# Kernel tuning notes

Hardware: AMD Instinct MI355X
Metric: run time of the kernel (lower is better)

The kernel has to match this reference:

```python
import jax, jax.numpy as jnp
import numpy as np

EPS = 1e-5


def setup_inputs() -> dict:
    key = jax.random.key(0)
    ks = jax.random.split(key, 6)
    B, C, H, W, K = 8, 512, 128, 128, 32
    x = jax.random.normal(ks[0], (B, C, H, W), jnp.float32)
    # 1x1 conv projection (ConvModule with BN -> no conv bias)
    conv_w = jax.random.normal(ks[1], (C, C), jnp.float32) * 0.02
    bn2_gamma = jnp.ones((C,), jnp.float32)
    bn2_beta = jnp.zeros((C,), jnp.float32)
    bn2_mean = jnp.zeros((C,), jnp.float32)
    bn2_var = jnp.ones((C,), jnp.float32)
    # Encoding: codewords [K, C], per-code smoothing scale [K]
    codewords = jax.random.normal(ks[2], (K, C), jnp.float32) * 0.1
    scale = -jax.random.uniform(ks[3], (K,), jnp.float32)  # negative scale as in mmcv init
    # BN1d over num_codes
    bn1_gamma = jnp.ones((K,), jnp.float32)
    bn1_beta = jnp.zeros((K,), jnp.float32)
    bn1_mean = jnp.zeros((K,), jnp.float32)
    bn1_var = jnp.ones((K,), jnp.float32)
    # channel-attention fc
    fc_w = jax.random.normal(ks[4], (C, C), jnp.float32) * 0.02
    fc_b = jnp.zeros((C,), jnp.float32)
    return {
        "x": x, "conv_w": conv_w,
        "bn2_gamma": bn2_gamma, "bn2_beta": bn2_beta, "bn2_mean": bn2_mean, "bn2_var": bn2_var,
        "codewords": codewords, "scale": scale,
        "bn1_gamma": bn1_gamma, "bn1_beta": bn1_beta, "bn1_mean": bn1_mean, "bn1_var": bn1_var,
        "fc_w": fc_w, "fc_b": fc_b,
    }


def reference(x, conv_w, bn2_gamma, bn2_beta, bn2_mean, bn2_var,
              codewords, scale, bn1_gamma, bn1_beta, bn1_mean, bn1_var,
              fc_w, fc_b):
    B, C, H, W = x.shape
    K = codewords.shape[0]
    # --- encoding_project: 1x1 conv + BN2d (eval) + ReLU ---
    p = jnp.einsum('bchw,oc->bohw', x, conv_w)
    inv2 = jax.lax.rsqrt(bn2_var + EPS)
    p = (p - bn2_mean[None, :, None, None]) * (inv2 * bn2_gamma)[None, :, None, None] \
        + bn2_beta[None, :, None, None]
    p = jax.nn.relu(p)
    # --- Encoding: scaled-L2 soft assignment + aggregation ---
    feat = p.reshape(B, C, H * W).transpose(0, 2, 1)          # [B, N, C]
    x2 = jnp.sum(feat * feat, axis=-1)                        # [B, N]
    c2 = jnp.sum(codewords * codewords, axis=-1)              # [K]
    xc = jnp.einsum('bnc,kc->bnk', feat, codewords)           # [B, N, K]
    scaled_l2 = scale[None, None, :] * (x2[:, :, None] - 2.0 * xc + c2[None, None, :])
    aw = jax.nn.softmax(scaled_l2, axis=2)                    # [B, N, K]
    # sum_n aw * (feat_n - c_k), without materializing [B,N,K,C]
    enc = jnp.einsum('bnk,bnc->bkc', aw, feat) \
        - jnp.sum(aw, axis=1)[:, :, None] * codewords[None]   # [B, K, C]
    # --- BN1d over codes (eval) + ReLU, then mean over codes ---
    inv1 = jax.lax.rsqrt(bn1_var + EPS)
    enc = (enc - bn1_mean[None, :, None]) * (inv1 * bn1_gamma)[None, :, None] \
        + bn1_beta[None, :, None]
    enc = jax.nn.relu(enc)
    encoding_feat = jnp.mean(enc, axis=1)                     # [B, C]
    # --- sigmoid channel gate + residual multiply-add + ReLU ---
    gamma = jax.nn.sigmoid(encoding_feat @ fc_w.T + fc_b)     # [B, C]
    output = jax.nn.relu(x + x * gamma[:, :, None, None])
    return (encoding_feat, output)
```

## Files before the change

kernel.cpp:

```cpp
#include <hip/hip_runtime.h>
#include <stdint.h>


#define EPSV 1e-5f

constexpr int Bn = 8, Cn = 512, Kn = 32, Nn = 16384;
constexpr int TILE_N = 64;
constexpr int NBLK = 256, BLK_PER_B = NBLK / Bn;
constexpr int TILES_PER_BLK = (Nn / TILE_N) / BLK_PER_B;

typedef float f32x4 __attribute__((ext_vector_type(4)));
typedef __bf16 bf16x8 __attribute__((ext_vector_type(8)));
union U4B8 { uint4 u; bf16x8 b; };

__device__ __forceinline__ uint32_t f2bf(float f) {
  uint32_t u = __float_as_uint(f);
  u += 0x7fffu + ((u >> 16) & 1u);
  return u >> 16;
}
__device__ __forceinline__ float bflo(uint32_t d) { return __uint_as_float(d << 16); }
__device__ __forceinline__ float bfhi(uint32_t d) { return __uint_as_float(d & 0xffff0000u); }

__global__ void k0_prep(const float* __restrict__ conv_w, const float* __restrict__ codewords,
                        const float* __restrict__ g2, const float* __restrict__ b2,
                        const float* __restrict__ m2, const float* __restrict__ v2,
                        uint16_t* __restrict__ WT2, uint16_t* __restrict__ cwb,
                        float* __restrict__ c2, float* __restrict__ bns, float* __restrict__ bnb)
{
  const int idx = blockIdx.x * blockDim.x + threadIdx.x;
  if (idx < Cn * Cn) {
    const int o = idx >> 9, c = idx & 511;
    const int cc = c >> 5, cl = c & 31;
    WT2[((size_t)cc * 512 + o) * 32 + cl] = (uint16_t)f2bf(conv_w[idx]);
  }
  if (idx < Kn * Cn) cwb[idx] = (uint16_t)f2bf(codewords[idx]);
  if (idx < Cn) {
    const float s = g2[idx] * rsqrtf(v2[idx] + EPSV);
    bns[idx] = s;
    bnb[idx] = b2[idx] - m2[idx] * s;
  }
  if (idx < Kn) {
    float s = 0.f;
    for (int c = 0; c < Cn; ++c) { const float v = codewords[idx * 512 + c]; s = fmaf(v, v, s); }
    c2[idx] = s;
  }
}

__launch_bounds__(512, 2)
__global__ void k1_main(const float* __restrict__ x,
                        const uint16_t* __restrict__ WT2,
                        const uint16_t* __restrict__ cwb,
                        const float* __restrict__ bns, const float* __restrict__ bnb,
                        const float* __restrict__ c2g, const float* __restrict__ scaleg,
                        float* __restrict__ encpart, float* __restrict__ awsumpart,
                        int parts)
{
  __shared__ __align__(16) uint32_t sP[512][33];
  __shared__ __align__(16) uint16_t sXF[64][520];
  __shared__ __align__(16) float    sAW[64][33];
  __shared__ float sX2[64];
  __shared__ float sBNs[512], sBNb[512];
  __shared__ float sScale[Kn], sC2[Kn];

  const int t    = threadIdx.x;
  const int lane = t & 63, w = t >> 6;
  const int col  = lane & 15, quad = lane >> 4;
  const int b    = blockIdx.x / BLK_PER_B;
  const int tb0  = blockIdx.x % BLK_PER_B;

  {
    sBNs[t] = bns[t];
    sBNb[t] = bnb[t];
    if (t < Kn) { sScale[t] = scaleg[t]; sC2[t] = c2g[t]; }
  }

  float enc[32];
#pragma unroll
  for (int u = 0; u < 32; ++u) enc[u] = 0.f;
  float awacc = 0.f;
  const int k_e3 = t & 31, cg = t >> 5;

  for (int j = 0; j < TILES_PER_BLK; ++j) {
    const int n0 = (tb0 + j * BLK_PER_B) * TILE_N;

    {
      const int c0 = t >> 4, n4 = (t & 15) * 4;
      const float* xp = x + ((size_t)(b * Cn) + c0) * Nn + n0 + n4;
      const int n2 = n4 >> 1;
#pragma unroll
      for (int i = 0; i < 16; ++i) {
        const float4 v = *(const float4*)(xp + (size_t)i * 32 * Nn);
        sP[c0 + i * 32][n2 + 0] = f2bf(v.x) | (f2bf(v.y) << 16);
        sP[c0 + i * 32][n2 + 1] = f2bf(v.z) | (f2bf(v.w) << 16);
      }
    }
    __syncthreads();

    {
      const int n = t & 63, seg = t >> 6;
      const int h = (n & 1) * 16, n2 = n >> 1;
#pragma unroll
      for (int u = 0; u < 8; ++u) {
        const int c0 = seg * 64 + u * 8;
        uint32_t o0, o1, o2, o3;
        {
          const uint32_t d0 = sP[c0 + 0][n2], d1 = sP[c0 + 1][n2];
          o0 = ((d0 >> h) & 0xffffu) | (((d1 >> h) & 0xffffu) << 16);
        }
        {
          const uint32_t d0 = sP[c0 + 2][n2], d1 = sP[c0 + 3][n2];
          o1 = ((d0 >> h) & 0xffffu) | (((d1 >> h) & 0xffffu) << 16);
        }
        {
          const uint32_t d0 = sP[c0 + 4][n2], d1 = sP[c0 + 5][n2];
          o2 = ((d0 >> h) & 0xffffu) | (((d1 >> h) & 0xffffu) << 16);
        }
        {
          const uint32_t d0 = sP[c0 + 6][n2], d1 = sP[c0 + 7][n2];
          o3 = ((d0 >> h) & 0xffffu) | (((d1 >> h) & 0xffffu) << 16);
        }
        *(uint4*)&sXF[n][c0] = make_uint4(o0, o1, o2, o3);
      }
    }
    __syncthreads();

    f32x4 acc[4][4];
#pragma unroll
    for (int ot = 0; ot < 4; ++ot)
#pragma unroll
      for (int nt = 0; nt < 4; ++nt) acc[ot][nt] = (f32x4){0.f, 0.f, 0.f, 0.f};

    {
      uint4 areg[2][4];
      const uint16_t* wbase = WT2 + (w * 64 + col) * 32 + quad * 8;
#pragma unroll
      for (int ot = 0; ot < 4; ++ot) areg[0][ot] = *(const uint4*)(wbase + ot * 512);
#pragma unroll
      for (int cc = 0; cc < 16; ++cc) {
        const int cur = cc & 1;
        if (cc + 1 < 16) {
          const uint16_t* wp = wbase + (size_t)(cc + 1) * 16384;
#pragma unroll
          for (int ot = 0; ot < 4; ++ot) areg[cur ^ 1][ot] = *(const uint4*)(wp + ot * 512);
        }
        U4B8 bfr[4];
#pragma unroll
        for (int nt = 0; nt < 4; ++nt)
          bfr[nt].u = *(const uint4*)&sXF[nt * 16 + col][cc * 32 + quad * 8];
#pragma unroll
        for (int ot = 0; ot < 4; ++ot) {
          U4B8 a; a.u = areg[cur][ot];
#pragma unroll
          for (int nt = 0; nt < 4; ++nt)
            acc[ot][nt] = __builtin_amdgcn_mfma_f32_16x16x32_bf16(a.b, bfr[nt].b, acc[ot][nt], 0, 0, 0);
        }
      }
    }
    __syncthreads();

#pragma unroll
    for (int ot = 0; ot < 4; ++ot) {
      const int ob = w * 64 + ot * 16 + quad * 4;
      const float4 s4 = *(const float4*)&sBNs[ob];
      const float4 b4 = *(const float4*)&sBNb[ob];
#pragma unroll
      for (int nt = 0; nt < 4; ++nt) {
        const f32x4 a = acc[ot][nt];
        const float r0 = fmaxf(fmaf(a[0], s4.x, b4.x), 0.f);
        const float r1 = fmaxf(fmaf(a[1], s4.y, b4.y), 0.f);
        const float r2 = fmaxf(fmaf(a[2], s4.z, b4.z), 0.f);
        const float r3 = fmaxf(fmaf(a[3], s4.w, b4.w), 0.f);
        *(uint2*)&sXF[nt * 16 + col][ob] = make_uint2(f2bf(r0) | (f2bf(r1) << 16),
                                                      f2bf(r2) | (f2bf(r3) << 16));
      }
    }
    __syncthreads();

    {
      const int n = t >> 3, cb = (t & 7) * 64;
      float s = 0.f;
#pragma unroll
      for (int u = 0; u < 8; ++u) {
        const uint4 d = *(const uint4*)&sXF[n][cb + u * 8];
        s = fmaf(bflo(d.x), bflo(d.x), s); s = fmaf(bfhi(d.x), bfhi(d.x), s);
        s = fmaf(bflo(d.y), bflo(d.y), s); s = fmaf(bfhi(d.y), bfhi(d.y), s);
        s = fmaf(bflo(d.z), bflo(d.z), s); s = fmaf(bfhi(d.z), bfhi(d.z), s);
        s = fmaf(bflo(d.w), bflo(d.w), s); s = fmaf(bfhi(d.w), bfhi(d.w), s);
      }
      s += __shfl_xor(s, 1); s += __shfl_xor(s, 2); s += __shfl_xor(s, 4);
      if ((t & 7) == 0) sX2[n] = s;
    }

    {
      const int kt = w & 1, ntl = w >> 1;
      f32x4 xca = (f32x4){0.f, 0.f, 0.f, 0.f};
      const uint16_t* cwp = cwb + (size_t)(kt * 16 + col) * 512 + quad * 8;
#pragma unroll
      for (int ks = 0; ks < 16; ++ks) {
        U4B8 af, bf;
        af.u = *(const uint4*)(cwp + ks * 32);
        bf.u = *(const uint4*)&sXF[ntl * 16 + col][ks * 32 + quad * 8];
        xca = __builtin_amdgcn_mfma_f32_16x16x32_bf16(af.b, bf.b, xca, 0, 0, 0);
      }
#pragma unroll
      for (int r = 0; r < 4; ++r)
        sAW[ntl * 16 + col][kt * 16 + quad * 4 + r] = xca[r];
    }
    __syncthreads();

    if (t < 64) {
      const float x2v = sX2[t];
      float m = -1e30f;
#pragma unroll
      for (int k = 0; k < Kn; ++k) {
        const float l = sScale[k] * (x2v - 2.f * sAW[t][k] + sC2[k]);
        sAW[t][k] = l;
        m = fmaxf(m, l);
      }
      float s = 0.f;
#pragma unroll
      for (int k = 0; k < Kn; ++k) { const float e = __expf(sAW[t][k] - m); sAW[t][k] = e; s += e; }
      const float inv = 1.f / s;
#pragma unroll
      for (int k = 0; k < Kn; ++k) sAW[t][k] *= inv;
    }
    __syncthreads();

#pragma unroll 2
    for (int n = 0; n < TILE_N; ++n) {
      const float a = sAW[n][k_e3];
      if (cg == 0) awacc += a;
      const uint16_t* fp = &sXF[n][cg * 32];
#pragma unroll
      for (int u = 0; u < 4; ++u) {
        const uint4 d = *(const uint4*)(fp + u * 8);
        enc[u*8+0] = fmaf(a, bflo(d.x), enc[u*8+0]);
        enc[u*8+1] = fmaf(a, bfhi(d.x), enc[u*8+1]);
        enc[u*8+2] = fmaf(a, bflo(d.y), enc[u*8+2]);
        enc[u*8+3] = fmaf(a, bfhi(d.y), enc[u*8+3]);
        enc[u*8+4] = fmaf(a, bflo(d.z), enc[u*8+4]);
        enc[u*8+5] = fmaf(a, bfhi(d.z), enc[u*8+5]);
        enc[u*8+6] = fmaf(a, bflo(d.w), enc[u*8+6]);
        enc[u*8+7] = fmaf(a, bfhi(d.w), enc[u*8+7]);
      }
    }
  }

  if (parts > 1) {
    float* dst = encpart + (((size_t)tb0 * Bn + b) * Kn + k_e3) * Cn + cg * 32;
#pragma unroll
    for (int u = 0; u < 8; ++u)
      *(float4*)(dst + u * 4) = make_float4(enc[u*4+0], enc[u*4+1], enc[u*4+2], enc[u*4+3]);
    if (cg == 0) awsumpart[((size_t)tb0 * Bn + b) * Kn + k_e3] = awacc;
  } else {
    float* dst = encpart + ((size_t)b * Kn + k_e3) * Cn + cg * 32;
#pragma unroll
    for (int u = 0; u < 32; ++u) atomicAdd(dst + u, enc[u]);
    if (cg == 0) atomicAdd(awsumpart + (size_t)b * Kn + k_e3, awacc);
  }
}

__global__ void k2a_reduce(float* __restrict__ encpart, int parts)
{
  const int b = blockIdx.x >> 5, s = blockIdx.x & 31;
  const int e0 = s * 512 + threadIdx.x;
#pragma unroll
  for (int r = 0; r < 2; ++r) {
    const size_t base = (size_t)b * (Kn * Cn) + e0 + r * 256;
    float v = encpart[base];
    for (int p = 1; p < parts; ++p)
      v += encpart[base + (size_t)p * (Bn * Kn * Cn)];
    encpart[base] = v;
  }
}

__global__ void k2_post(const float* __restrict__ encpart, const float* __restrict__ awsumpart,
                        const float* __restrict__ codewords,
                        const float* __restrict__ g1, const float* __restrict__ b1,
                        const float* __restrict__ m1, const float* __restrict__ v1,
                        const float* __restrict__ fc_w, const float* __restrict__ fc_b,
                        float* __restrict__ ef_out, float* __restrict__ gamma,
                        int parts)
{
  __shared__ float efs[Cn];
  __shared__ float saws[Kn];
  const int b = blockIdx.x, c = threadIdx.x;

  if (c < Kn) {
    float s = 0.f;
    for (int p = 0; p < parts; ++p) s += awsumpart[((size_t)p * Bn + b) * Kn + c];
    saws[c] = s;
  }
  __syncthreads();

  float s = 0.f;
#pragma unroll 4
  for (int k = 0; k < Kn; ++k) {
    float e = encpart[((size_t)b * Kn + k) * Cn + c] - saws[k] * codewords[k * Cn + c];
    const float inv = rsqrtf(v1[k] + EPSV);
    e = (e - m1[k]) * (inv * g1[k]) + b1[k];
    s += fmaxf(e, 0.f);
  }
  s *= (1.f / 32.f);
  efs[c] = s;
  ef_out[b * Cn + c] = s;
  __syncthreads();
  const float4* w4 = (const float4*)(fc_w + (size_t)c * Cn);
  const float4* e4 = (const float4*)efs;
  float z = 0.f;
#pragma unroll 8
  for (int i = 0; i < Cn / 4; ++i) {
    const float4 w = w4[i], e = e4[i];
    z = fmaf(w.x, e.x, z); z = fmaf(w.y, e.y, z);
    z = fmaf(w.z, e.z, z); z = fmaf(w.w, e.w, z);
  }
  z += fc_b[c];
  gamma[b * Cn + c] = 1.f / (1.f + __expf(-z));
}

__global__ void k3_out(const float* __restrict__ x, const float* __restrict__ gamma,
                       float* __restrict__ out)
{
  const float4* x4 = (const float4*)x;
  float4* o4 = (float4*)out;
  int i = blockIdx.x * blockDim.x + threadIdx.x;
#pragma unroll
  for (int r = 0; r < 8; ++r, i += 2097152) {
    const int bb = i >> 21;
    const int cc = (i >> 12) & 511;
    const float g = 1.f + gamma[bb * 512 + cc];
    float4 v = x4[i];
    v.x = fmaxf(v.x * g, 0.f);
    v.y = fmaxf(v.y * g, 0.f);
    v.z = fmaxf(v.z * g, 0.f);
    v.w = fmaxf(v.w * g, 0.f);
    o4[i] = v;
  }
}

extern "C" void kernel_launch(void* const* d_in, const int* in_sizes, int n_in,
                              void* d_out, int out_size, void* d_ws, size_t ws_size,
                              hipStream_t stream) {
  const float* x      = (const float*)d_in[0];
  const float* conv_w = (const float*)d_in[1];
  const float* bn2g   = (const float*)d_in[2];
  const float* bn2b   = (const float*)d_in[3];
  const float* bn2m   = (const float*)d_in[4];
  const float* bn2v   = (const float*)d_in[5];
  const float* codew  = (const float*)d_in[6];
  const float* scale  = (const float*)d_in[7];
  const float* bn1g   = (const float*)d_in[8];
  const float* bn1b   = (const float*)d_in[9];
  const float* bn1m   = (const float*)d_in[10];
  const float* bn1v   = (const float*)d_in[11];
  const float* fc_w   = (const float*)d_in[12];
  const float* fc_b   = (const float*)d_in[13];

  const size_t enc_part_bytes = (size_t)BLK_PER_B * Bn * Kn * Cn * 4;
  const size_t aws_part_bytes = (size_t)BLK_PER_B * Bn * Kn * 4;
  const size_t enc_fall_bytes = (size_t)Bn * Kn * Cn * 4;
  const size_t aws_fall_bytes = (size_t)Bn * Kn * 4;
  const size_t fixed_bytes = (size_t)Bn * Cn * 4
                           + (size_t)Cn * Cn * 2
                           + (size_t)Kn * Cn * 2
                           + (size_t)Kn * 4
                           + (size_t)Cn * 4
                           + (size_t)Cn * 4;
  const bool use_parts = ws_size >= enc_part_bytes + aws_part_bytes + fixed_bytes;
  const int parts = use_parts ? BLK_PER_B : 1;
  const size_t enc_bytes = use_parts ? enc_part_bytes : enc_fall_bytes;
  const size_t aws_bytes = use_parts ? aws_part_bytes : aws_fall_bytes;

  char* ws = (char*)d_ws;
  float*    encpart  = (float*)ws;                       ws += enc_bytes;
  float*    awsumpart= (float*)ws;                       ws += aws_bytes;
  float*    gamma    = (float*)ws;                       ws += (size_t)Bn * Cn * 4;
  uint16_t* WT2      = (uint16_t*)ws;                    ws += (size_t)Cn * Cn * 2;
  uint16_t* cwb      = (uint16_t*)ws;                    ws += (size_t)Kn * Cn * 2;
  float*    c2       = (float*)ws;                       ws += (size_t)Kn * 4;
  float*    bns      = (float*)ws;                       ws += (size_t)Cn * 4;
  float*    bnb      = (float*)ws;

  if (!use_parts)
    hipMemsetAsync(encpart, 0, enc_bytes + aws_bytes, stream);

  k0_prep<<<1024, 256, 0, stream>>>(conv_w, codew, bn2g, bn2b, bn2m, bn2v,
                                    WT2, cwb, c2, bns, bnb);
  k1_main<<<NBLK, 512, 0, stream>>>(x, WT2, cwb, bns, bnb, c2, scale,
                                    encpart, awsumpart, parts);
  if (parts > 1)
    k2a_reduce<<<256, 256, 0, stream>>>(encpart, parts);
  k2_post<<<Bn, Cn, 0, stream>>>(encpart, awsumpart, codew, bn1g, bn1b, bn1m, bn1v,
                                 fc_w, fc_b, (float*)d_out, gamma, parts);
  k3_out<<<8192, 256, 0, stream>>>(x, gamma, (float*)d_out + Bn * Cn);
}
```

Before: 999.1 us.

## Drop staging LDS buffer, load x directly transposed, raise occupancy and grid size

Removes the sP staging buffer and its second transpose pass: each thread now reads scalar x values along N for four channels and writes packed bf16 pairs straight into sXF. This frees about 67KB of LDS, so launch bounds go from 2 to 4 blocks per CU and the grid can grow to 512 blocks with 64 partial slices when the workspace allows. The cost is scalar instead of float4 global loads, a larger partial-sum buffer and a heavier reduction. A leading __syncthreads is added per tile to guard sXF reuse.

```diff
diff --git a/kernel.cpp b/kernel.cpp
--- a/kernel.cpp
+++ b/kernel.cpp
@@ -6,8 +6,7 @@
 
 constexpr int Bn = 8, Cn = 512, Kn = 32, Nn = 16384;
 constexpr int TILE_N = 64;
-constexpr int NBLK = 256, BLK_PER_B = NBLK / Bn;
-constexpr int TILES_PER_BLK = (Nn / TILE_N) / BLK_PER_B;
+constexpr int NTILES = Nn / TILE_N;
 
 typedef float f32x4 __attribute__((ext_vector_type(4)));
 typedef __bf16 bf16x8 __attribute__((ext_vector_type(8)));
@@ -46,16 +45,15 @@
   }
 }
 
-__launch_bounds__(512, 2)
+__launch_bounds__(512, 4)
 __global__ void k1_main(const float* __restrict__ x,
                         const uint16_t* __restrict__ WT2,
                         const uint16_t* __restrict__ cwb,
                         const float* __restrict__ bns, const float* __restrict__ bnb,
                         const float* __restrict__ c2g, const float* __restrict__ scaleg,
                         float* __restrict__ encpart, float* __restrict__ awsumpart,
-                        int parts)
-{
-  __shared__ __align__(16) uint32_t sP[512][33];
+                        int parts, int lgBPB)
+{
   __shared__ __align__(16) uint16_t sXF[64][520];
   __shared__ __align__(16) float    sAW[64][33];
   __shared__ float sX2[64];
@@ -65,8 +63,9 @@
   const int t    = threadIdx.x;
   const int lane = t & 63, w = t >> 6;
   const int col  = lane & 15, quad = lane >> 4;
-  const int b    = blockIdx.x / BLK_PER_B;
-  const int tb0  = blockIdx.x % BLK_PER_B;
+  const int b    = blockIdx.x >> lgBPB;
+  const int tb0  = blockIdx.x & ((1 << lgBPB) - 1);
+  const int tiles = NTILES >> lgBPB;
 
   {
     sBNs[t] = bns[t];
@@ -80,46 +79,23 @@
   float awacc = 0.f;
   const int k_e3 = t & 31, cg = t >> 5;
 
-  for (int j = 0; j < TILES_PER_BLK; ++j) {
-    const int n0 = (tb0 + j * BLK_PER_B) * TILE_N;
+  for (int j = 0; j < tiles; ++j) {
+    const int n0 = (tb0 + (j << lgBPB)) * TILE_N;
+
+    __syncthreads();
 
     {
-      const int c0 = t >> 4, n4 = (t & 15) * 4;
-      const float* xp = x + ((size_t)(b * Cn) + c0) * Nn + n0 + n4;
-      const int n2 = n4 >> 1;
-#pragma unroll
-      for (int i = 0; i < 16; ++i) {
-        const float4 v = *(const float4*)(xp + (size_t)i * 32 * Nn);
-        sP[c0 + i * 32][n2 + 0] = f2bf(v.x) | (f2bf(v.y) << 16);
-        sP[c0 + i * 32][n2 + 1] = f2bf(v.z) | (f2bf(v.w) << 16);
-      }
-    }
-    __syncthreads();
-
-    {
-      const int n = t & 63, seg = t >> 6;
-      const int h = (n & 1) * 16, n2 = n >> 1;
-#pragma unroll
-      for (int u = 0; u < 8; ++u) {
-        const int c0 = seg * 64 + u * 8;
-        uint32_t o0, o1, o2, o3;
-        {
-          const uint32_t d0 = sP[c0 + 0][n2], d1 = sP[c0 + 1][n2];
-          o0 = ((d0 >> h) & 0xffffu) | (((d1 >> h) & 0xffffu) << 16);
-        }
-        {
-          const uint32_t d0 = sP[c0 + 2][n2], d1 = sP[c0 + 3][n2];
-          o1 = ((d0 >> h) & 0xffffu) | (((d1 >> h) & 0xffffu) << 16);
-        }
-        {
-          const uint32_t d0 = sP[c0 + 4][n2], d1 = sP[c0 + 5][n2];
-          o2 = ((d0 >> h) & 0xffffu) | (((d1 >> h) & 0xffffu) << 16);
-        }
-        {
-          const uint32_t d0 = sP[c0 + 6][n2], d1 = sP[c0 + 7][n2];
-          o3 = ((d0 >> h) & 0xffffu) | (((d1 >> h) & 0xffffu) << 16);
-        }
-        *(uint4*)&sXF[n][c0] = make_uint4(o0, o1, o2, o3);
+      const float* xb = x + (size_t)b * Cn * Nn + n0 + lane;
+#pragma unroll
+      for (int p = 0; p < 16; ++p) {
+        const int c0 = w * 64 + p * 4;
+        const float* xp = xb + (size_t)c0 * Nn;
+        const float v0 = xp[0];
+        const float v1 = xp[(size_t)Nn];
+        const float v2 = xp[(size_t)2 * Nn];
+        const float v3 = xp[(size_t)3 * Nn];
+        *(uint2*)&sXF[lane][c0] = make_uint2(f2bf(v0) | (f2bf(v1) << 16),
+                                             f2bf(v2) | (f2bf(v3) << 16));
       }
     }
     __syncthreads();
@@ -356,20 +332,24 @@
   const float* fc_w   = (const float*)d_in[12];
   const float* fc_b   = (const float*)d_in[13];
 
-  const size_t enc_part_bytes = (size_t)BLK_PER_B * Bn * Kn * Cn * 4;
-  const size_t aws_part_bytes = (size_t)BLK_PER_B * Bn * Kn * 4;
-  const size_t enc_fall_bytes = (size_t)Bn * Kn * Cn * 4;
-  const size_t aws_fall_bytes = (size_t)Bn * Kn * 4;
   const size_t fixed_bytes = (size_t)Bn * Cn * 4
                            + (size_t)Cn * Cn * 2
                            + (size_t)Kn * Cn * 2
                            + (size_t)Kn * 4
                            + (size_t)Cn * 4
                            + (size_t)Cn * 4;
-  const bool use_parts = ws_size >= enc_part_bytes + aws_part_bytes + fixed_bytes;
-  const int parts = use_parts ? BLK_PER_B : 1;
-  const size_t enc_bytes = use_parts ? enc_part_bytes : enc_fall_bytes;
-  const size_t aws_bytes = use_parts ? aws_part_bytes : aws_fall_bytes;
+  const size_t enc64 = (size_t)64 * Bn * Kn * Cn * 4;
+  const size_t aws64 = (size_t)64 * Bn * Kn * 4;
+  const size_t enc32 = (size_t)32 * Bn * Kn * Cn * 4;
+  const size_t aws32 = (size_t)32 * Bn * Kn * 4;
+  const size_t enc1  = (size_t)Bn * Kn * Cn * 4;
+  const size_t aws1  = (size_t)Bn * Kn * 4;
+
+  int parts, lgBPB, nblk;
+  size_t enc_bytes, aws_bytes;
+  if (ws_size >= enc64 + aws64 + fixed_bytes)      { parts = 64; lgBPB = 6; nblk = 512; enc_bytes = enc64; aws_bytes = aws64; }
+  else if (ws_size >= enc32 + aws32 + fixed_bytes) { parts = 32; lgBPB = 5; nblk = 256; enc_bytes = enc32; aws_bytes = aws32; }
+  else                                             { parts = 1;  lgBPB = 5; nblk = 256; enc_bytes = enc1;  aws_bytes = aws1;  }
 
   char* ws = (char*)d_ws;
   float*    encpart  = (float*)ws;                       ws += enc_bytes;
@@ -381,13 +361,13 @@
   float*    bns      = (float*)ws;                       ws += (size_t)Cn * 4;
   float*    bnb      = (float*)ws;
 
-  if (!use_parts)
+  if (parts == 1)
     hipMemsetAsync(encpart, 0, enc_bytes + aws_bytes, stream);
 
   k0_prep<<<1024, 256, 0, stream>>>(conv_w, codew, bn2g, bn2b, bn2m, bn2v,
                                     WT2, cwb, c2, bns, bnb);
-  k1_main<<<NBLK, 512, 0, stream>>>(x, WT2, cwb, bns, bnb, c2, scale,
-                                    encpart, awsumpart, parts);
+  k1_main<<<nblk, 512, 0, stream>>>(x, WT2, cwb, bns, bnb, c2, scale,
+                                    encpart, awsumpart, parts, lgBPB);
   if (parts > 1)
     k2a_reduce<<<256, 256, 0, stream>>>(encpart, parts);
   k2_post<<<Bn, Cn, 0, stream>>>(encpart, awsumpart, codew, bn1g, bn1b, bn1m, bn1v,
```

Measured after the change: 1.115 ms. 1.12x slower.
